# Performance work log

Hardware: AMD Instinct MI355X
Metric: run time of the kernel (lower is better)

The kernel has to match this reference:

```python
import jax, jax.numpy as jnp
import numpy as np

N_NODES = 200000
N_EDGES = 600000
N_GRAPHS = 4000
EMB = 128
LAYERS = 5
TASKS = 128
ATOM_FEATS, ATOM_VOCAB = 9, 64
BOND_FEATS, BOND_VOCAB = 3, 8
BN_EPS = 1e-5


def setup_inputs() -> dict:
    key = jax.random.key(0)
    ks = jax.random.split(key, 16)
    x = jax.random.randint(ks[0], (N_NODES, ATOM_FEATS), 0, ATOM_VOCAB)
    edge_index = jax.random.randint(ks[1], (2, N_EDGES), 0, N_NODES)
    edge_attr = jax.random.randint(ks[2], (N_EDGES, BOND_FEATS), 0, BOND_VOCAB)
    batch = jnp.sort(jax.random.randint(ks[3], (N_NODES,), 0, N_GRAPHS))
    s = 1.0 / np.sqrt(EMB)
    atom_emb = jax.random.normal(ks[4], (ATOM_FEATS, ATOM_VOCAB, EMB), jnp.float32) * s
    bond_emb = jax.random.normal(ks[5], (LAYERS, BOND_FEATS, BOND_VOCAB, EMB), jnp.float32) * s
    W = jax.random.normal(ks[6], (LAYERS, EMB, EMB), jnp.float32) * s
    b = jax.random.normal(ks[7], (LAYERS, EMB), jnp.float32) * 0.01
    root = jax.random.normal(ks[8], (LAYERS, EMB), jnp.float32) * s
    bn_mean = jax.random.normal(ks[9], (LAYERS, EMB), jnp.float32) * 0.1
    bn_var = jax.random.uniform(ks[10], (LAYERS, EMB), jnp.float32, 0.5, 1.5)
    bn_gamma = jax.random.uniform(ks[11], (LAYERS, EMB), jnp.float32, 0.5, 1.5)
    bn_beta = jax.random.normal(ks[12], (LAYERS, EMB), jnp.float32) * 0.1
    headW = jax.random.normal(ks[13], (EMB, TASKS), jnp.float32) * s
    headb = jnp.zeros((TASKS,), jnp.float32)
    return {"x": x, "edge_index": edge_index, "edge_attr": edge_attr, "batch": batch,
            "atom_emb": atom_emb, "bond_emb": bond_emb, "W": W, "b": b, "root": root,
            "bn_mean": bn_mean, "bn_var": bn_var, "bn_gamma": bn_gamma, "bn_beta": bn_beta,
            "headW": headW, "headb": headb}


def _gcn_forward(x, edge_index, edge_attr, batch, atom_emb, bond_emb, W, b, root,
                 bn_mean, bn_var, bn_gamma, bn_beta, headW, headb):
    src, dst = edge_index[0], edge_index[1]
    # AtomEncoder: sum of per-feature embeddings  -> [N, EMB]
    h = jnp.sum(jnp.take_along_axis(atom_emb, x.T[:, :, None], axis=1).squeeze(2), axis=0) \
        if False else sum(atom_emb[f][x[:, f]] for f in range(ATOM_FEATS))
    # degree of source nodes (+1 self loop), as in OGB GCNConv
    deg = jnp.zeros((N_NODES,), h.dtype).at[src].add(1.0) + 1.0
    dinv = deg ** -0.5
    norm = dinv[src] * dinv[dst]  # [E]
    for l in range(LAYERS):
        xl = h @ W[l] + b[l]
        edge_emb = sum(bond_emb[l, f][edge_attr[:, f]] for f in range(BOND_FEATS))  # [E, EMB]
        msg = norm[:, None] * jax.nn.relu(xl[src] + edge_emb)
        agg = jax.ops.segment_sum(msg, dst, num_segments=N_NODES)
        h = agg + jax.nn.relu(xl + root[l]) / deg[:, None]
        # BatchNorm1d (eval mode: running stats)
        h = (h - bn_mean[l]) * (bn_gamma[l] / jnp.sqrt(bn_var[l] + BN_EPS)) + bn_beta[l]
        if l != LAYERS - 1:
            h = jax.nn.relu(h)
        # dropout is identity in eval mode
    # global_add_pool over graphs
    hg = jax.ops.segment_sum(h, batch, num_segments=N_GRAPHS)
    return hg @ headW + headb


def reference(x, edge_index, edge_attr, batch, atom_emb, bond_emb, W, b, root,
              bn_mean, bn_var, bn_gamma, bn_beta, headW, headb):
    return _gcn_forward(x, edge_index, edge_attr, batch, atom_emb, bond_emb, W, b, root,
                        bn_mean, bn_var, bn_gamma, bn_beta, headW, headb)
```

## Files before the change

### kernel.cpp

```cpp
#include <hip/hip_runtime.h>
#include <hip/hip_bf16.h>

#define N_NODES 200000
#define N_EDGES 600000
#define N_GRAPHS 4000
#define EMB 128
#define LAYERS 5
#define BN_EPS 1e-5f

#define SCAN_CHUNK 2048
#define N_CHUNKS ((N_NODES + SCAN_CHUNK - 1) / SCAN_CHUNK)

typedef __attribute__((ext_vector_type(8))) short short8;
typedef __attribute__((ext_vector_type(8))) unsigned short ushort8v;
typedef __attribute__((ext_vector_type(4))) float float4v;

__device__ __forceinline__ void bf16split(float f, unsigned short& hi, unsigned short& lo) {
    unsigned u = __float_as_uint(f);
    hi = (unsigned short)(u >> 16);
    float hf = __uint_as_float((unsigned)hi << 16);
    lo = (unsigned short)(__float_as_uint(f - hf) >> 16);
}

__device__ __forceinline__ unsigned short f2bf_rne(float f) {
    unsigned u = __float_as_uint(f);
    u += 0x7FFF + ((u >> 16) & 1);
    return (unsigned short)(u >> 16);
}
__device__ __forceinline__ float bf2f(unsigned short h) {
    return __uint_as_float((unsigned)h << 16);
}

#define CNT_BLOCKS 2344
#define WP_BASE   CNT_BLOCKS
#define WP_BLOCKS 320
#define CB_BASE   (WP_BASE + WP_BLOCKS)
#define CB_BLOCKS 1280
#define BN_BASE   (CB_BASE + CB_BLOCKS)
#define BN_BLOCKS 3
#define GB_BASE   (BN_BASE + BN_BLOCKS)
#define GB_BLOCKS 16
#define AB_BASE   (GB_BASE + GB_BLOCKS)
#define AB_BLOCKS 288
#define PREP_BLOCKS (AB_BASE + AB_BLOCKS)

__global__ __launch_bounds__(256) void prep_all(
    const int* __restrict__ ei_src, const int* __restrict__ ei_dst,
    int* __restrict__ dsrc, int* __restrict__ ddst,
    const float* __restrict__ W, unsigned short* __restrict__ whi,
    unsigned short* __restrict__ wlo,
    const float* __restrict__ bemb, unsigned short* __restrict__ combo,
    const float* __restrict__ mean, const float* __restrict__ var,
    const float* __restrict__ gamma, const float* __restrict__ beta,
    float* __restrict__ S, float* __restrict__ T,
    const int* __restrict__ batch, int* __restrict__ gptr,
    const float* __restrict__ aemb, unsigned short* __restrict__ aembb) {
    const int b = blockIdx.x, tid = threadIdx.x;
    if (b < CNT_BLOCKS) {
        const int e = b * 256 + tid;
        if (e < N_EDGES) {
            atomicAdd(&dsrc[ei_src[e]], 1);
            atomicAdd(&ddst[ei_dst[e]], 1);
        }
    } else if (b < CB_BASE) {
        const int idx = (b - WP_BASE) * 256 + tid;
        const int l = idx >> 14, rem = idx & 16383;
        const int k = rem >> 7, n = rem & 127;
        unsigned short hi, lo;
        bf16split(W[idx], hi, lo);
        const int off = (l << 14) + ((((k >> 5) * 8 + (n >> 4)) * 64
                        + ((k >> 3) & 3) * 16 + (n & 15)) << 3) + (k & 7);
        whi[off] = hi;
        wlo[off] = lo;
    } else if (b < BN_BASE) {
        const int idx = (b - CB_BASE) * 256 + tid;
        const int l = idx >> 16;
        const int c = (idx >> 7) & 511;
        const int ch = idx & 127;
        const int a0 = c & 7, a1 = (c >> 3) & 7, a2 = c >> 6;
        combo[(size_t)(l * 512 + c) * EMB + ch] = f2bf_rne(
            bemb[(size_t)((l * 3 + 0) * 8 + a0) * EMB + ch] +
            bemb[(size_t)((l * 3 + 1) * 8 + a1) * EMB + ch] +
            bemb[(size_t)((l * 3 + 2) * 8 + a2) * EMB + ch]);
    } else if (b < GB_BASE) {
        const int i = (b - BN_BASE) * 256 + tid;
        if (i < LAYERS * EMB) {
            float s = gamma[i] / sqrtf(var[i] + BN_EPS);
            S[i] = s;
            T[i] = beta[i] - mean[i] * s;
        }
    } else if (b < AB_BASE) {
        const int g = (b - GB_BASE) * 256 + tid;
        if (g > N_GRAPHS) return;
        if (g == N_GRAPHS) { gptr[g] = N_NODES; return; }
        int lo = 0, hi = N_NODES;
        while (lo < hi) {
            int mid = (lo + hi) >> 1;
            if (batch[mid] < g) lo = mid + 1; else hi = mid;
        }
        gptr[g] = lo;
    } else {
        const int idx = (b - AB_BASE) * 256 + tid;
        aembb[idx] = f2bf_rne(aemb[idx]);
    }
}

__global__ __launch_bounds__(256) void scan1(const int* __restrict__ deg, int* __restrict__ partial) {
    __shared__ int sd[256];
    const int base = blockIdx.x * SCAN_CHUNK + threadIdx.x * 8;
    int s = 0;
#pragma unroll
    for (int i = 0; i < 8; ++i) { int idx = base + i; s += (idx < N_NODES) ? deg[idx] : 0; }
    sd[threadIdx.x] = s; __syncthreads();
    for (int off = 128; off > 0; off >>= 1) {
        if (threadIdx.x < off) sd[threadIdx.x] += sd[threadIdx.x + off];
        __syncthreads();
    }
    if (threadIdx.x == 0) partial[blockIdx.x] = sd[0];
}

__global__ __launch_bounds__(256) void scan3(const int* __restrict__ deg,
                                             const int* __restrict__ partial,
                                             int* __restrict__ rowptr) {
    __shared__ int sd[256];
    __shared__ int base_off;
    const int tid = threadIdx.x;
    if (tid == 0) {
        int acc = 0;
        for (int i = 0; i < (int)blockIdx.x; ++i) acc += partial[i];
        base_off = acc;
    }
    const int base = blockIdx.x * SCAN_CHUNK + tid * 8;
    int loc[8]; int s = 0;
#pragma unroll
    for (int i = 0; i < 8; ++i) { int idx = base + i; loc[i] = (idx < N_NODES) ? deg[idx] : 0; s += loc[i]; }
    sd[tid] = s; __syncthreads();
    for (int off = 1; off < 256; off <<= 1) {
        int v = (tid >= off) ? sd[tid - off] : 0;
        __syncthreads();
        sd[tid] += v;
        __syncthreads();
    }
    int excl = base_off + sd[tid] - s;
#pragma unroll
    for (int i = 0; i < 8; ++i) {
        int idx = base + i;
        if (idx < N_NODES) { rowptr[idx] = excl; excl += loc[i]; }
    }
    if (blockIdx.x == 0 && tid == 0) rowptr[N_NODES] = N_EDGES;
}

__global__ void scatter_k(const int* __restrict__ srcs, const int* __restrict__ dsts,
                          const int* __restrict__ eattr, const int* __restrict__ dsrc,
                          const int* __restrict__ rowptr, int* __restrict__ fill,
                          int* __restrict__ epk, float* __restrict__ enrm) {
    int e = blockIdx.x * blockDim.x + threadIdx.x;
    if (e >= N_EDGES) return;
    const int s = srcs[e];
    const int d = dsts[e];
    const int pos = rowptr[d] + atomicAdd(&fill[d], 1);
    const int c = eattr[e * 3] | (eattr[e * 3 + 1] << 3) | (eattr[e * 3 + 2] << 6);
    epk[pos] = s | (c << 18);
    enrm[pos] = rsqrtf((float)(dsrc[s] + 1) * (float)(dsrc[d] + 1));
}

__device__ __forceinline__ void mfma_tile64(
    unsigned short (*AhAl)[64][136],
    const short8* __restrict__ Bh, const short8* __restrict__ Bl,
    const float* __restrict__ bias, unsigned short* __restrict__ XLout,
    size_t rows, int tid) {
    const int wave = tid >> 6;
    const int lane = tid & 63;
    const int quad = lane >> 4;
    const int n15  = lane & 15;
    const int rt   = wave & 3;
    const int cp   = wave >> 2;
    const int arow = rt * 16 + n15;

    float4v acc0 = (float4v)(0.f);
    float4v acc1 = (float4v)(0.f);
#pragma unroll
    for (int ks = 0; ks < 4; ++ks) {
        const int k0 = ks * 32 + quad * 8;
        const short8 ah = *(const short8*)&AhAl[0][arow][k0];
        const short8 al = *(const short8*)&AhAl[1][arow][k0];
        const short8 bh0 = Bh[(ks * 8 + cp * 2 + 0) * 64 + lane];
        const short8 bl0 = Bl[(ks * 8 + cp * 2 + 0) * 64 + lane];
        const short8 bh1 = Bh[(ks * 8 + cp * 2 + 1) * 64 + lane];
        const short8 bl1 = Bl[(ks * 8 + cp * 2 + 1) * 64 + lane];
        acc0 = __builtin_amdgcn_mfma_f32_16x16x32_bf16(ah, bh0, acc0, 0, 0, 0);
        acc0 = __builtin_amdgcn_mfma_f32_16x16x32_bf16(ah, bl0, acc0, 0, 0, 0);
        acc0 = __builtin_amdgcn_mfma_f32_16x16x32_bf16(al, bh0, acc0, 0, 0, 0);
        acc1 = __builtin_amdgcn_mfma_f32_16x16x32_bf16(ah, bh1, acc1, 0, 0, 0);
        acc1 = __builtin_amdgcn_mfma_f32_16x16x32_bf16(ah, bl1, acc1, 0, 0, 0);
        acc1 = __builtin_amdgcn_mfma_f32_16x16x32_bf16(al, bh1, acc1, 0, 0, 0);
    }

    const size_t rowBase = rows + rt * 16 + quad * 4;
    const int col0 = (cp * 2 + 0) * 16 + n15;
    const int col1 = (cp * 2 + 1) * 16 + n15;
    const float bc0 = bias[col0];
    const float bc1 = bias[col1];
#pragma unroll
    for (int r = 0; r < 4; ++r) {
        XLout[(rowBase + r) * EMB + col0] = f2bf_rne(acc0[r] + bc0);
        XLout[(rowBase + r) * EMB + col1] = f2bf_rne(acc1[r] + bc1);
    }
}

__device__ __forceinline__ void mfma_tile16(
    unsigned short (*AhAl)[16][136],
    const short8* __restrict__ Bh, const short8* __restrict__ Bl,
    const float* __restrict__ bias, unsigned short* __restrict__ XLout,
    size_t rows, int tid) {
    const int wave = tid >> 6;
    const int lane = tid & 63;
    const int quad = lane >> 4;
    const int n15  = lane & 15;
    const int cp   = wave;
    const int arow = n15;

    float4v acc0 = (float4v)(0.f);
    float4v acc1 = (float4v)(0.f);
#pragma unroll
    for (int ks = 0; ks < 4; ++ks) {
        const int k0 = ks * 32 + quad * 8;
        const short8 ah = *(const short8*)&AhAl[0][arow][k0];
        const short8 al = *(const short8*)&AhAl[1][arow][k0];
        const short8 bh0 = Bh[(ks * 8 + cp * 2 + 0) * 64 + lane];
        const short8 bl0 = Bl[(ks * 8 + cp * 2 + 0) * 64 + lane];
        const short8 bh1 = Bh[(ks * 8 + cp * 2 + 1) * 64 + lane];
        const short8 bl1 = Bl[(ks * 8 + cp * 2 + 1) * 64 + lane];
        acc0 = __builtin_amdgcn_mfma_f32_16x16x32_bf16(ah, bh0, acc0, 0, 0, 0);
        acc0 = __builtin_amdgcn_mfma_f32_16x16x32_bf16(ah, bl0, acc0, 0, 0, 0);
        acc0 = __builtin_amdgcn_mfma_f32_16x16x32_bf16(al, bh0, acc0, 0, 0, 0);
        acc1 = __builtin_amdgcn_mfma_f32_16x16x32_bf16(ah, bh1, acc1, 0, 0, 0);
        acc1 = __builtin_amdgcn_mfma_f32_16x16x32_bf16(ah, bl1, acc1, 0, 0, 0);
        acc1 = __builtin_amdgcn_mfma_f32_16x16x32_bf16(al, bh1, acc1, 0, 0, 0);
    }

    const size_t rowBase = rows + quad * 4;
    const int col0 = (cp * 2 + 0) * 16 + n15;
    const int col1 = (cp * 2 + 1) * 16 + n15;
    const float bc0 = bias[col0];
    const float bc1 = bias[col1];
#pragma unroll
    for (int r = 0; r < 4; ++r) {
        XLout[(rowBase + r) * EMB + col0] = f2bf_rne(acc0[r] + bc0);
        XLout[(rowBase + r) * EMB + col1] = f2bf_rne(acc1[r] + bc1);
    }
}

__global__ __launch_bounds__(1024, 8) void enc_gemm(
    const int* __restrict__ x, const unsigned short* __restrict__ aembb,
    const unsigned short* __restrict__ whi, const unsigned short* __restrict__ wlo,
    const float* __restrict__ bias, unsigned short* __restrict__ XL) {
    __shared__ unsigned short AhAl[2][64][136];
    const int tid = threadIdx.x;
    const int q = tid & 15, qw = tid >> 4;
    const int c0 = q * 8;
    const size_t rows = (size_t)blockIdx.x * 64;

    {
        const size_t n = rows + qw;
        float4 a0 = make_float4(0.f, 0.f, 0.f, 0.f), a1 = a0;
#pragma unroll
        for (int ff = 0; ff < 9; ++ff) {
            const int v = x[n * 9 + ff];
            const ushort8v e = *(const ushort8v*)&aembb[(size_t)(ff * 64 + v) * EMB + c0];
            a0.x += bf2f(e[0]); a0.y += bf2f(e[1]);
            a0.z += bf2f(e[2]); a0.w += bf2f(e[3]);
            a1.x += bf2f(e[4]); a1.y += bf2f(e[5]);
            a1.z += bf2f(e[6]); a1.w += bf2f(e[7]);
        }
        ushort4 hi, lo;
        bf16split(a0.x, hi.x, lo.x); bf16split(a0.y, hi.y, lo.y);
        bf16split(a0.z, hi.z, lo.z); bf16split(a0.w, hi.w, lo.w);
        *(ushort4*)&AhAl[0][qw][c0] = hi;
        *(ushort4*)&AhAl[1][qw][c0] = lo;
        bf16split(a1.x, hi.x, lo.x); bf16split(a1.y, hi.y, lo.y);
        bf16split(a1.z, hi.z, lo.z); bf16split(a1.w, hi.w, lo.w);
        *(ushort4*)&AhAl[0][qw][c0 + 4] = hi;
        *(ushort4*)&AhAl[1][qw][c0 + 4] = lo;
    }
    __syncthreads();
    mfma_tile64(AhAl, (const short8*)whi, (const short8*)wlo, bias, XL, rows, tid);
}

__global__ __launch_bounds__(256, 8) void gather_gemm(
    const int* __restrict__ rowptr, const int* __restrict__ epk,
    const float* __restrict__ enrm, const unsigned short* __restrict__ combo,
    const float* __restrict__ root, const int* __restrict__ dsrc,
    const float* __restrict__ bnS, const float* __restrict__ bnT,
    const unsigned short* __restrict__ whi, const unsigned short* __restrict__ wlo,
    const float* __restrict__ bias,
    const unsigned short* __restrict__ XLin, unsigned short* __restrict__ XLout) {
    __shared__ unsigned short AhAl[2][16][136];
    const int tid = threadIdx.x;
    const int q = tid & 15, qw = tid >> 4;
    const int c0 = q * 8;
    const size_t rows = (size_t)blockIdx.x * 16;

    {
        const size_t n = rows + qw;
        const float4 r40 = *(const float4*)&root[c0];
        const float4 r41 = *(const float4*)&root[c0 + 4];
        const float4 s40 = *(const float4*)&bnS[c0];
        const float4 s41 = *(const float4*)&bnS[c0 + 4];
        const float4 t40 = *(const float4*)&bnT[c0];
        const float4 t41 = *(const float4*)&bnT[c0 + 4];
        const float dinv = 1.0f / (float)(dsrc[n] + 1);
        const ushort8v xn = *(const ushort8v*)&XLin[n * EMB + c0];
        float4 a0, a1;
        a0.x = fmaxf(bf2f(xn[0]) + r40.x, 0.f) * dinv;
        a0.y = fmaxf(bf2f(xn[1]) + r40.y, 0.f) * dinv;
        a0.z = fmaxf(bf2f(xn[2]) + r40.z, 0.f) * dinv;
        a0.w = fmaxf(bf2f(xn[3]) + r40.w, 0.f) * dinv;
        a1.x = fmaxf(bf2f(xn[4]) + r41.x, 0.f) * dinv;
        a1.y = fmaxf(bf2f(xn[5]) + r41.y, 0.f) * dinv;
        a1.z = fmaxf(bf2f(xn[6]) + r41.z, 0.f) * dinv;
        a1.w = fmaxf(bf2f(xn[7]) + r41.w, 0.f) * dinv;

        const int beg = rowptr[n], end = rowptr[n + 1];
        int pk = 0; float wgt = 0.f;
        if (beg < end) { pk = epk[beg]; wgt = enrm[beg]; }
        for (int e = beg; e < end; ++e) {
            const int pk_c = pk; const float w_c = wgt;
            if (e + 1 < end) { pk = epk[e + 1]; wgt = enrm[e + 1]; }
            const size_t sb = (size_t)(pk_c & 0x3FFFF) * EMB + c0;
            const size_t cbx = (size_t)(pk_c >> 18) * EMB + c0;
            const ushort8v xv = *(const ushort8v*)&XLin[sb];
            const ushort8v cb = *(const ushort8v*)&combo[cbx];
            a0.x += fmaxf(bf2f(xv[0]) + bf2f(cb[0]), 0.f) * w_c;
            a0.y += fmaxf(bf2f(xv[1]) + bf2f(cb[1]), 0.f) * w_c;
            a0.z += fmaxf(bf2f(xv[2]) + bf2f(cb[2]), 0.f) * w_c;
            a0.w += fmaxf(bf2f(xv[3]) + bf2f(cb[3]), 0.f) * w_c;
            a1.x += fmaxf(bf2f(xv[4]) + bf2f(cb[4]), 0.f) * w_c;
            a1.y += fmaxf(bf2f(xv[5]) + bf2f(cb[5]), 0.f) * w_c;
            a1.z += fmaxf(bf2f(xv[6]) + bf2f(cb[6]), 0.f) * w_c;
            a1.w += fmaxf(bf2f(xv[7]) + bf2f(cb[7]), 0.f) * w_c;
        }
        float4 h0, h1;
        h0.x = fmaxf(fmaf(a0.x, s40.x, t40.x), 0.f);
        h0.y = fmaxf(fmaf(a0.y, s40.y, t40.y), 0.f);
        h0.z = fmaxf(fmaf(a0.z, s40.z, t40.z), 0.f);
        h0.w = fmaxf(fmaf(a0.w, s40.w, t40.w), 0.f);
        h1.x = fmaxf(fmaf(a1.x, s41.x, t41.x), 0.f);
        h1.y = fmaxf(fmaf(a1.y, s41.y, t41.y), 0.f);
        h1.z = fmaxf(fmaf(a1.z, s41.z, t41.z), 0.f);
        h1.w = fmaxf(fmaf(a1.w, s41.w, t41.w), 0.f);
        ushort4 hi, lo;
        bf16split(h0.x, hi.x, lo.x); bf16split(h0.y, hi.y, lo.y);
        bf16split(h0.z, hi.z, lo.z); bf16split(h0.w, hi.w, lo.w);
        *(ushort4*)&AhAl[0][qw][c0] = hi;
        *(ushort4*)&AhAl[1][qw][c0] = lo;
        bf16split(h1.x, hi.x, lo.x); bf16split(h1.y, hi.y, lo.y);
        bf16split(h1.z, hi.z, lo.z); bf16split(h1.w, hi.w, lo.w);
        *(ushort4*)&AhAl[0][qw][c0 + 4] = hi;
        *(ushort4*)&AhAl[1][qw][c0 + 4] = lo;
    }
    __syncthreads();
    mfma_tile16(AhAl, (const short8*)whi, (const short8*)wlo, bias, XLout, rows, tid);
}

__global__ __launch_bounds__(512) void gather_pool_head(
    const int* __restrict__ rowptr, const int* __restrict__ epk,
    const float* __restrict__ enrm, const unsigned short* __restrict__ combo,
    const float* __restrict__ root, const int* __restrict__ dsrc,
    const float* __restrict__ S4, const float* __restrict__ T4,
    const int* __restrict__ gptr, const unsigned short* __restrict__ XLin,
    const float* __restrict__ HW, const float* __restrict__ hb,
    float* __restrict__ OUT) {
    __shared__ float red[32][EMB];
    __shared__ float hr[EMB];
    const int gph = blockIdx.x;
    const int q = threadIdx.x & 15, qw = threadIdx.x >> 4;
    const int c0 = q * 8;
    const int nbeg = gptr[gph], nend = gptr[gph + 1];
    const int ebeg = rowptr[nbeg], eend = rowptr[nend];

    const float4 r40 = *(const float4*)&root[c0];
    const float4 r41 = *(const float4*)&root[c0 + 4];

    float4 seg0 = make_float4(0.f, 0.f, 0.f, 0.f), seg1 = seg0;
    for (int n = nbeg + qw; n < nend; n += 32) {
        const float dinv = 1.0f / (float)(dsrc[n] + 1);
        const ushort8v xn = *(const ushort8v*)&XLin[(size_t)n * EMB + c0];
        seg0.x += fmaxf(bf2f(xn[0]) + r40.x, 0.f) * dinv;
        seg0.y += fmaxf(bf2f(xn[1]) + r40.y, 0.f) * dinv;
        seg0.z += fmaxf(bf2f(xn[2]) + r40.z, 0.f) * dinv;
        seg0.w += fmaxf(bf2f(xn[3]) + r40.w, 0.f) * dinv;
        seg1.x += fmaxf(bf2f(xn[4]) + r41.x, 0.f) * dinv;
        seg1.y += fmaxf(bf2f(xn[5]) + r41.y, 0.f) * dinv;
        seg1.z += fmaxf(bf2f(xn[6]) + r41.z, 0.f) * dinv;
        seg1.w += fmaxf(bf2f(xn[7]) + r41.w, 0.f) * dinv;
    }
    for (int i = ebeg + qw; i < eend; i += 32) {
        const int pk = epk[i];
        const float w = enrm[i];
        const size_t sb = (size_t)(pk & 0x3FFFF) * EMB + c0;
        const size_t cbx = (size_t)(pk >> 18) * EMB + c0;
        const ushort8v xv = *(const ushort8v*)&XLin[sb];
        const ushort8v cb = *(const ushort8v*)&combo[cbx];
        seg0.x += fmaxf(bf2f(xv[0]) + bf2f(cb[0]), 0.f) * w;
        seg0.y += fmaxf(bf2f(xv[1]) + bf2f(cb[1]), 0.f) * w;
        seg0.z += fmaxf(bf2f(xv[2]) + bf2f(cb[2]), 0.f) * w;
        seg0.w += fmaxf(bf2f(xv[3]) + bf2f(cb[3]), 0.f) * w;
        seg1.x += fmaxf(bf2f(xv[4]) + bf2f(cb[4]), 0.f) * w;
        seg1.y += fmaxf(bf2f(xv[5]) + bf2f(cb[5]), 0.f) * w;
        seg1.z += fmaxf(bf2f(xv[6]) + bf2f(cb[6]), 0.f) * w;
        seg1.w += fmaxf(bf2f(xv[7]) + bf2f(cb[7]), 0.f) * w;
    }
    *(float4*)&red[qw][c0] = seg0;
    *(float4*)&red[qw][c0 + 4] = seg1;
    __syncthreads();

    const int t = threadIdx.x;
    if (t < EMB) {
        float v = 0.f;
#pragma unroll
        for (int r = 0; r < 32; ++r) v += red[r][t];
        hr[t] = fmaf(v, S4[t], T4[t] * (float)(nend - nbeg));
    }
    __syncthreads();
    if (t < EMB) {
        float o = hb[t];
#pragma unroll 8
        for (int k = 0; k < EMB; ++k) o = fmaf(hr[k], HW[(size_t)k * EMB + t], o);
        OUT[(size_t)gph * EMB + t] = o;
    }
}

extern "C" void kernel_launch(void* const* d_in, const int* in_sizes, int n_in,
                              void* d_out, int out_size, void* d_ws, size_t ws_size,
                              hipStream_t stream) {
    const int*   x     = (const int*)d_in[0];
    const int*   ei    = (const int*)d_in[1];
    const int*   ea    = (const int*)d_in[2];
    const int*   batch = (const int*)d_in[3];
    const float* aemb  = (const float*)d_in[4];
    const float* bemb  = (const float*)d_in[5];
    const float* W     = (const float*)d_in[6];
    const float* b     = (const float*)d_in[7];
    const float* root  = (const float*)d_in[8];
    const float* bnm   = (const float*)d_in[9];
    const float* bnv   = (const float*)d_in[10];
    const float* bng   = (const float*)d_in[11];
    const float* bnb   = (const float*)d_in[12];
    const float* hW    = (const float*)d_in[13];
    const float* hb    = (const float*)d_in[14];
    float* out = (float*)d_out;

    const size_t NF = (size_t)N_NODES * EMB;
    const size_t n_float = NF + (size_t)LAYERS * 512 * EMB / 2
                         + 2 * LAYERS * EMB + N_EDGES
                         + 2 * ((size_t)LAYERS * 16384 / 2 + 64)
                         + (9 * 64 * EMB / 2 + 64);
    const size_t n_int   = 3 * (size_t)N_NODES + (N_NODES + 4) + 128
                         + (N_GRAPHS + 4) + N_EDGES;
    const size_t need = (n_float + n_int) * sizeof(float);
    if (ws_size < need) return;

    float* f     = (float*)d_ws;
    unsigned short* bufA = (unsigned short*)f; f += NF / 2;
    unsigned short* bufB = (unsigned short*)f; f += NF / 2;
    unsigned short* combo = (unsigned short*)f; f += (size_t)LAYERS * 512 * EMB / 2;
    float* S     = f;                          f += LAYERS * EMB;
    float* T     = f;                          f += LAYERS * EMB;
    float* enrm  = f;                          f += N_EDGES;
    unsigned short* whi = (unsigned short*)f;  f += (size_t)LAYERS * 16384 / 2 + 64;
    unsigned short* wlo = (unsigned short*)f;  f += (size_t)LAYERS * 16384 / 2 + 64;
    unsigned short* aembb = (unsigned short*)f; f += 9 * 64 * EMB / 2 + 64;
    int*   ip    = (int*)f;
    int*   dsrc    = ip;                       ip += N_NODES;
    int*   ddst    = ip;                       ip += N_NODES;
    int*   fill    = ip;                       ip += N_NODES;
    int*   rowptr  = ip;                       ip += N_NODES + 4;
    int*   partial = ip;                       ip += 128;
    int*   gptr    = ip;                       ip += N_GRAPHS + 4;
    int*   epk     = ip;                       ip += N_EDGES;

    hipMemsetAsync(dsrc, 0, 3 * (size_t)N_NODES * sizeof(int), stream);

    prep_all<<<PREP_BLOCKS, 256, 0, stream>>>(
        ei, ei + N_EDGES, dsrc, ddst, W, whi, wlo, bemb, combo,
        bnm, bnv, bng, bnb, S, T, batch, gptr, aemb, aembb);
    scan1<<<N_CHUNKS, 256, 0, stream>>>(ddst, partial);
    scan3<<<N_CHUNKS, 256, 0, stream>>>(ddst, partial, rowptr);
    scatter_k<<<(N_EDGES + 255) / 256, 256, 0, stream>>>(ei, ei + N_EDGES, ea, dsrc,
                                                         rowptr, fill, epk, enrm);

    enc_gemm<<<N_NODES / 64, 1024, 0, stream>>>(x, aembb, whi, wlo, b, bufA);

    unsigned short* in    = bufA;
    unsigned short* other = bufB;
    for (int l = 0; l < 4; ++l) {
        gather_gemm<<<N_NODES / 16, 256, 0, stream>>>(
            rowptr, epk, enrm, combo + (size_t)l * 512 * EMB, root + l * EMB, dsrc,
            S + l * EMB, T + l * EMB,
            whi + (size_t)(l + 1) * 16384, wlo + (size_t)(l + 1) * 16384,
            b + (l + 1) * EMB, in, other);
        unsigned short* t0 = in; in = other; other = t0;
    }

    gather_pool_head<<<N_GRAPHS, 512, 0, stream>>>(
        rowptr, epk, enrm, combo + (size_t)4 * 512 * EMB, root + 4 * EMB, dsrc,
        S + 4 * EMB, T + 4 * EMB, gptr, in, hW, hb, out);
}
```

Baseline: 544.5 us.

## Pack edge records into int2 and halve gather_gemm block to 128 threads

Edge source/attribute code and normalization weight are now stored together as one int2 record, so each edge needs a single 8-byte load instead of two separate array reads. The gather_gemm kernel now uses 128 threads per 16-row tile. Each thread covers 16 columns with two 16-byte loads per edge, and each of the two waves computes four 16-column MFMA tiles instead of two. The aim is fewer threads and fewer index loads per node, at the cost of more registers per thread and less parallelism per block.

```diff
diff --git a/kernel.cpp b/kernel.cpp
--- a/kernel.cpp
+++ b/kernel.cpp
@@ -153,15 +153,15 @@
 __global__ void scatter_k(const int* __restrict__ srcs, const int* __restrict__ dsts,
                           const int* __restrict__ eattr, const int* __restrict__ dsrc,
                           const int* __restrict__ rowptr, int* __restrict__ fill,
-                          int* __restrict__ epk, float* __restrict__ enrm) {
+                          int2* __restrict__ erec) {
     int e = blockIdx.x * blockDim.x + threadIdx.x;
     if (e >= N_EDGES) return;
     const int s = srcs[e];
     const int d = dsts[e];
     const int pos = rowptr[d] + atomicAdd(&fill[d], 1);
     const int c = eattr[e * 3] | (eattr[e * 3 + 1] << 3) | (eattr[e * 3 + 2] << 6);
-    epk[pos] = s | (c << 18);
-    enrm[pos] = rsqrtf((float)(dsrc[s] + 1) * (float)(dsrc[d] + 1));
+    const float nrm = rsqrtf((float)(dsrc[s] + 1) * (float)(dsrc[d] + 1));
+    erec[pos] = make_int2(s | (c << 18), __float_as_int(nrm));
 }
 
 __device__ __forceinline__ void mfma_tile64(
@@ -208,7 +208,7 @@
     }
 }
 
-__device__ __forceinline__ void mfma_tile16(
+__device__ __forceinline__ void mfma_tile16w2(
     unsigned short (*AhAl)[16][136],
     const short8* __restrict__ Bh, const short8* __restrict__ Bl,
     const float* __restrict__ bias, unsigned short* __restrict__ XLout,
@@ -217,37 +217,36 @@
     const int lane = tid & 63;
     const int quad = lane >> 4;
     const int n15  = lane & 15;
-    const int cp   = wave;
     const int arow = n15;
 
-    float4v acc0 = (float4v)(0.f);
-    float4v acc1 = (float4v)(0.f);
+    float4v acc[4];
+#pragma unroll
+    for (int j = 0; j < 4; ++j) acc[j] = (float4v)(0.f);
+
 #pragma unroll
     for (int ks = 0; ks < 4; ++ks) {
         const int k0 = ks * 32 + quad * 8;
         const short8 ah = *(const short8*)&AhAl[0][arow][k0];
         const short8 al = *(const short8*)&AhAl[1][arow][k0];
-        const short8 bh0 = Bh[(ks * 8 + cp * 2 + 0) * 64 + lane];
-        const short8 bl0 = Bl[(ks * 8 + cp * 2 + 0) * 64 + lane];
-        const short8 bh1 = Bh[(ks * 8 + cp * 2 + 1) * 64 + lane];
-        const short8 bl1 = Bl[(ks * 8 + cp * 2 + 1) * 64 + lane];
-        acc0 = __builtin_amdgcn_mfma_f32_16x16x32_bf16(ah, bh0, acc0, 0, 0, 0);
-        acc0 = __builtin_amdgcn_mfma_f32_16x16x32_bf16(ah, bl0, acc0, 0, 0, 0);
-        acc0 = __builtin_amdgcn_mfma_f32_16x16x32_bf16(al, bh0, acc0, 0, 0, 0);
-        acc1 = __builtin_amdgcn_mfma_f32_16x16x32_bf16(ah, bh1, acc1, 0, 0, 0);
-        acc1 = __builtin_amdgcn_mfma_f32_16x16x32_bf16(ah, bl1, acc1, 0, 0, 0);
-        acc1 = __builtin_amdgcn_mfma_f32_16x16x32_bf16(al, bh1, acc1, 0, 0, 0);
+#pragma unroll
+        for (int j = 0; j < 4; ++j) {
+            const int ct = wave * 4 + j;
+            const short8 bh = Bh[(ks * 8 + ct) * 64 + lane];
+            const short8 bl = Bl[(ks * 8 + ct) * 64 + lane];
+            acc[j] = __builtin_amdgcn_mfma_f32_16x16x32_bf16(ah, bh, acc[j], 0, 0, 0);
+            acc[j] = __builtin_amdgcn_mfma_f32_16x16x32_bf16(ah, bl, acc[j], 0, 0, 0);
+            acc[j] = __builtin_amdgcn_mfma_f32_16x16x32_bf16(al, bh, acc[j], 0, 0, 0);
+        }
     }
 
     const size_t rowBase = rows + quad * 4;
-    const int col0 = (cp * 2 + 0) * 16 + n15;
-    const int col1 = (cp * 2 + 1) * 16 + n15;
-    const float bc0 = bias[col0];
-    const float bc1 = bias[col1];
-#pragma unroll
-    for (int r = 0; r < 4; ++r) {
-        XLout[(rowBase + r) * EMB + col0] = f2bf_rne(acc0[r] + bc0);
-        XLout[(rowBase + r) * EMB + col1] = f2bf_rne(acc1[r] + bc1);
+#pragma unroll
+    for (int j = 0; j < 4; ++j) {
+        const int col = (wave * 4 + j) * 16 + n15;
+        const float bc = bias[col];
+#pragma unroll
+        for (int r = 0; r < 4; ++r)
+            XLout[(rowBase + r) * EMB + col] = f2bf_rne(acc[j][r] + bc);
     }
 }
 
@@ -287,9 +286,9 @@
     mfma_tile64(AhAl, (const short8*)whi, (const short8*)wlo, bias, XL, rows, tid);
 }
 
-__global__ __launch_bounds__(256, 8) void gather_gemm(
-    const int* __restrict__ rowptr, const int* __restrict__ epk,
-    const float* __restrict__ enrm, const unsigned short* __restrict__ combo,
+__global__ __launch_bounds__(128, 8) void gather_gemm(
+    const int* __restrict__ rowptr, const int2* __restrict__ erec,
+    const unsigned short* __restrict__ combo,
     const float* __restrict__ root, const int* __restrict__ dsrc,
     const float* __restrict__ bnS, const float* __restrict__ bnT,
     const unsigned short* __restrict__ whi, const unsigned short* __restrict__ wlo,
@@ -297,75 +296,113 @@
     const unsigned short* __restrict__ XLin, unsigned short* __restrict__ XLout) {
     __shared__ unsigned short AhAl[2][16][136];
     const int tid = threadIdx.x;
-    const int q = tid & 15, qw = tid >> 4;
-    const int c0 = q * 8;
+    const int o = tid & 7, qw = tid >> 3;
+    const int c0 = o * 16;
     const size_t rows = (size_t)blockIdx.x * 16;
 
     {
         const size_t n = rows + qw;
-        const float4 r40 = *(const float4*)&root[c0];
-        const float4 r41 = *(const float4*)&root[c0 + 4];
-        const float4 s40 = *(const float4*)&bnS[c0];
-        const float4 s41 = *(const float4*)&bnS[c0 + 4];
-        const float4 t40 = *(const float4*)&bnT[c0];
-        const float4 t41 = *(const float4*)&bnT[c0 + 4];
         const float dinv = 1.0f / (float)(dsrc[n] + 1);
-        const ushort8v xn = *(const ushort8v*)&XLin[n * EMB + c0];
-        float4 a0, a1;
-        a0.x = fmaxf(bf2f(xn[0]) + r40.x, 0.f) * dinv;
-        a0.y = fmaxf(bf2f(xn[1]) + r40.y, 0.f) * dinv;
-        a0.z = fmaxf(bf2f(xn[2]) + r40.z, 0.f) * dinv;
-        a0.w = fmaxf(bf2f(xn[3]) + r40.w, 0.f) * dinv;
-        a1.x = fmaxf(bf2f(xn[4]) + r41.x, 0.f) * dinv;
-        a1.y = fmaxf(bf2f(xn[5]) + r41.y, 0.f) * dinv;
-        a1.z = fmaxf(bf2f(xn[6]) + r41.z, 0.f) * dinv;
-        a1.w = fmaxf(bf2f(xn[7]) + r41.w, 0.f) * dinv;
+        float4 a0, a1, a2, a3;
+        {
+            const ushort8v xn0 = *(const ushort8v*)&XLin[n * EMB + c0];
+            const ushort8v xn1 = *(const ushort8v*)&XLin[n * EMB + c0 + 8];
+            const float4 r0 = *(const float4*)&root[c0];
+            const float4 r1 = *(const float4*)&root[c0 + 4];
+            const float4 r2 = *(const float4*)&root[c0 + 8];
+            const float4 r3 = *(const float4*)&root[c0 + 12];
+            a0.x = fmaxf(bf2f(xn0[0]) + r0.x, 0.f) * dinv;
+            a0.y = fmaxf(bf2f(xn0[1]) + r0.y, 0.f) * dinv;
+            a0.z = fmaxf(bf2f(xn0[2]) + r0.z, 0.f) * dinv;
+            a0.w = fmaxf(bf2f(xn0[3]) + r0.w, 0.f) * dinv;
+            a1.x = fmaxf(bf2f(xn0[4]) + r1.x, 0.f) * dinv;
+            a1.y = fmaxf(bf2f(xn0[5]) + r1.y, 0.f) * dinv;
+            a1.z = fmaxf(bf2f(xn0[6]) + r1.z, 0.f) * dinv;
+            a1.w = fmaxf(bf2f(xn0[7]) + r1.w, 0.f) * dinv;
+            a2.x = fmaxf(bf2f(xn1[0]) + r2.x, 0.f) * dinv;
+            a2.y = fmaxf(bf2f(xn1[1]) + r2.y, 0.f) * dinv;
+            a2.z = fmaxf(bf2f(xn1[2]) + r2.z, 0.f) * dinv;
+            a2.w = fmaxf(bf2f(xn1[3]) + r2.w, 0.f) * dinv;
+            a3.x = fmaxf(bf2f(xn1[4]) + r3.x, 0.f) * dinv;
+            a3.y = fmaxf(bf2f(xn1[5]) + r3.y, 0.f) * dinv;
+            a3.z = fmaxf(bf2f(xn1[6]) + r3.z, 0.f) * dinv;
+            a3.w = fmaxf(bf2f(xn1[7]) + r3.w, 0.f) * dinv;
+        }
 
         const int beg = rowptr[n], end = rowptr[n + 1];
-        int pk = 0; float wgt = 0.f;
-        if (beg < end) { pk = epk[beg]; wgt = enrm[beg]; }
+        int2 rec = make_int2(0, 0);
+        if (beg < end) rec = erec[beg];
         for (int e = beg; e < end; ++e) {
-            const int pk_c = pk; const float w_c = wgt;
-            if (e + 1 < end) { pk = epk[e + 1]; wgt = enrm[e + 1]; }
-            const size_t sb = (size_t)(pk_c & 0x3FFFF) * EMB + c0;
-            const size_t cbx = (size_t)(pk_c >> 18) * EMB + c0;
-            const ushort8v xv = *(const ushort8v*)&XLin[sb];
-            const ushort8v cb = *(const ushort8v*)&combo[cbx];
-            a0.x += fmaxf(bf2f(xv[0]) + bf2f(cb[0]), 0.f) * w_c;
-            a0.y += fmaxf(bf2f(xv[1]) + bf2f(cb[1]), 0.f) * w_c;
-            a0.z += fmaxf(bf2f(xv[2]) + bf2f(cb[2]), 0.f) * w_c;
-            a0.w += fmaxf(bf2f(xv[3]) + bf2f(cb[3]), 0.f) * w_c;
-            a1.x += fmaxf(bf2f(xv[4]) + bf2f(cb[4]), 0.f) * w_c;
-            a1.y += fmaxf(bf2f(xv[5]) + bf2f(cb[5]), 0.f) * w_c;
-            a1.z += fmaxf(bf2f(xv[6]) + bf2f(cb[6]), 0.f) * w_c;
-            a1.w += fmaxf(bf2f(xv[7]) + bf2f(cb[7]), 0.f) * w_c;
-        }
-        float4 h0, h1;
-        h0.x = fmaxf(fmaf(a0.x, s40.x, t40.x), 0.f);
-        h0.y = fmaxf(fmaf(a0.y, s40.y, t40.y), 0.f);
-        h0.z = fmaxf(fmaf(a0.z, s40.z, t40.z), 0.f);
-        h0.w = fmaxf(fmaf(a0.w, s40.w, t40.w), 0.f);
-        h1.x = fmaxf(fmaf(a1.x, s41.x, t41.x), 0.f);
-        h1.y = fmaxf(fmaf(a1.y, s41.y, t41.y), 0.f);
-        h1.z = fmaxf(fmaf(a1.z, s41.z, t41.z), 0.f);
-        h1.w = fmaxf(fmaf(a1.w, s41.w, t41.w), 0.f);
+            const int pk = rec.x;
+            const float w = __int_as_float(rec.y);
+            if (e + 1 < end) rec = erec[e + 1];
+            const size_t sb = (size_t)(pk & 0x3FFFF) * EMB + c0;
+            const size_t cbx = (size_t)(pk >> 18) * EMB + c0;
+            const ushort8v xv0 = *(const ushort8v*)&XLin[sb];
+            const ushort8v xv1 = *(const ushort8v*)&XLin[sb + 8];
+            const ushort8v cb0 = *(const ushort8v*)&combo[cbx];
+            const ushort8v cb1 = *(const ushort8v*)&combo[cbx + 8];
+            a0.x += fmaxf(bf2f(xv0[0]) + bf2f(cb0[0]), 0.f) * w;
+            a0.y += fmaxf(bf2f(xv0[1]) + bf2f(cb0[1]), 0.f) * w;
+            a0.z += fmaxf(bf2f(xv0[2]) + bf2f(cb0[2]), 0.f) * w;
+            a0.w += fmaxf(bf2f(xv0[3]) + bf2f(cb0[3]), 0.f) * w;
+            a1.x += fmaxf(bf2f(xv0[4]) + bf2f(cb0[4]), 0.f) * w;
+            a1.y += fmaxf(bf2f(xv0[5]) + bf2f(cb0[5]), 0.f) * w;
+            a1.z += fmaxf(bf2f(xv0[6]) + bf2f(cb0[6]), 0.f) * w;
+            a1.w += fmaxf(bf2f(xv0[7]) + bf2f(cb0[7]), 0.f) * w;
+            a2.x += fmaxf(bf2f(xv1[0]) + bf2f(cb1[0]), 0.f) * w;
+            a2.y += fmaxf(bf2f(xv1[1]) + bf2f(cb1[1]), 0.f) * w;
+            a2.z += fmaxf(bf2f(xv1[2]) + bf2f(cb1[2]), 0.f) * w;
+            a2.w += fmaxf(bf2f(xv1[3]) + bf2f(cb1[3]), 0.f) * w;
+            a3.x += fmaxf(bf2f(xv1[4]) + bf2f(cb1[4]), 0.f) * w;
+            a3.y += fmaxf(bf2f(xv1[5]) + bf2f(cb1[5]), 0.f) * w;
+            a3.z += fmaxf(bf2f(xv1[6]) + bf2f(cb1[6]), 0.f) * w;
+            a3.w += fmaxf(bf2f(xv1[7]) + bf2f(cb1[7]), 0.f) * w;
+        }
+
+        const float4 s0 = *(const float4*)&bnS[c0];
+        const float4 s1 = *(const float4*)&bnS[c0 + 4];
+        const float4 s2 = *(const float4*)&bnS[c0 + 8];
+        const float4 s3 = *(const float4*)&bnS[c0 + 12];
+        const float4 t0 = *(const float4*)&bnT[c0];
+        const float4 t1 = *(const float4*)&bnT[c0 + 4];
+        const float4 t2 = *(const float4*)&bnT[c0 + 8];
+        const float4 t3 = *(const float4*)&bnT[c0 + 12];
+        float h[16];
+        h[0]  = fmaxf(fmaf(a0.x, s0.x, t0.x), 0.f);
+        h[1]  = fmaxf(fmaf(a0.y, s0.y, t0.y), 0.f);
+        h[2]  = fmaxf(fmaf(a0.z, s0.z, t0.z), 0.f);
+        h[3]  = fmaxf(fmaf(a0.w, s0.w, t0.w), 0.f);
+        h[4]  = fmaxf(fmaf(a1.x, s1.x, t1.x), 0.f);
+        h[5]  = fmaxf(fmaf(a1.y, s1.y, t1.y), 0.f);
+        h[6]  = fmaxf(fmaf(a1.z, s1.z, t1.z), 0.f);
+        h[7]  = fmaxf(fmaf(a1.w, s1.w, t1.w), 0.f);
+        h[8]  = fmaxf(fmaf(a2.x, s2.x, t2.x), 0.f);
+        h[9]  = fmaxf(fmaf(a2.y, s2.y, t2.y), 0.f);
+        h[10] = fmaxf(fmaf(a2.z, s2.z, t2.z), 0.f);
+        h[11] = fmaxf(fmaf(a2.w, s2.w, t2.w), 0.f);
+        h[12] = fmaxf(fmaf(a3.x, s3.x, t3.x), 0.f);
+        h[13] = fmaxf(fmaf(a3.y, s3.y, t3.y), 0.f);
+        h[14] = fmaxf(fmaf(a3.z, s3.z, t3.z), 0.f);
+        h[15] = fmaxf(fmaf(a3.w, s3.w, t3.w), 0.f);
         ushort4 hi, lo;
-        bf16split(h0.x, hi.x, lo.x); bf16split(h0.y, hi.y, lo.y);
-        bf16split(h0.z, hi.z, lo.z); bf16split(h0.w, hi.w, lo.w);
-        *(ushort4*)&AhAl[0][qw][c0] = hi;
-        *(ushort4*)&AhAl[1][qw][c0] = lo;
-        bf16split(h1.x, hi.x, lo.x); bf16split(h1.y, hi.y, lo.y);
-        bf16split(h1.z, hi.z, lo.z); bf16split(h1.w, hi.w, lo.w);
-        *(ushort4*)&AhAl[0][qw][c0 + 4] = hi;
-        *(ushort4*)&AhAl[1][qw][c0 + 4] = lo;
+#pragma unroll
+        for (int g4 = 0; g4 < 4; ++g4) {
+            bf16split(h[g4 * 4 + 0], hi.x, lo.x);
+            bf16split(h[g4 * 4 + 1], hi.y, lo.y);
+            bf16split(h[g4 * 4 + 2], hi.z, lo.z);
+            bf16split(h[g4 * 4 + 3], hi.w, lo.w);
+            *(ushort4*)&AhAl[0][qw][c0 + g4 * 4] = hi;
+            *(ushort4*)&AhAl[1][qw][c0 + g4 * 4] = lo;
+        }
     }
     __syncthreads();
-    mfma_tile16(AhAl, (const short8*)whi, (const short8*)wlo, bias, XLout, rows, tid);
+    mfma_tile16w2(AhAl, (const short8*)whi, (const short8*)wlo, bias, XLout, rows, tid);
 }
 
 __global__ __launch_bounds__(512) void gather_pool_head(
-    const int* __restrict__ rowptr, const int* __restrict__ epk,
-    const float* __restrict__ enrm, const unsigned short* __restrict__ combo,
+    const int* __restrict__ rowptr, const int2* __restrict__ erec,
+    const unsigned short* __restrict__ combo,
     const float* __restrict__ root, const int* __restrict__ dsrc,
     const float* __restrict__ S4, const float* __restrict__ T4,
     const int* __restrict__ gptr, const unsigned short* __restrict__ XLin,
@@ -396,8 +433,9 @@
         seg1.w += fmaxf(bf2f(xn[7]) + r41.w, 0.f) * dinv;
     }
     for (int i = ebeg + qw; i < eend; i += 32) {
-        const int pk = epk[i];
-        const float w = enrm[i];
+        const int2 rec = erec[i];
+        const int pk = rec.x;
+        const float w = __int_as_float(rec.y);
         const size_t sb = (size_t)(pk & 0x3FFFF) * EMB + c0;
         const size_t cbx = (size_t)(pk >> 18) * EMB + c0;
         const ushort8v xv = *(const ushort8v*)&XLin[sb];
@@ -453,11 +491,12 @@
 
     const size_t NF = (size_t)N_NODES * EMB;
     const size_t n_float = NF + (size_t)LAYERS * 512 * EMB / 2
-                         + 2 * LAYERS * EMB + N_EDGES
+                         + 2 * LAYERS * EMB
                          + 2 * ((size_t)LAYERS * 16384 / 2 + 64)
                          + (9 * 64 * EMB / 2 + 64);
-    const size_t n_int   = 3 * (size_t)N_NODES + (N_NODES + 4) + 128
-                         + (N_GRAPHS + 4) + N_EDGES;
+    const size_t n_int   = 2 * (size_t)N_EDGES
+                         + 3 * (size_t)N_NODES + (N_NODES + 4) + 128
+                         + (N_GRAPHS + 4);
     const size_t need = (n_float + n_int) * sizeof(float);
     if (ws_size < need) return;
 
@@ -467,18 +506,17 @@
     unsigned short* combo = (unsigned short*)f; f += (size_t)LAYERS * 512 * EMB / 2;
     float* S     = f;                          f += LAYERS * EMB;
     float* T     = f;                          f += LAYERS * EMB;
-    float* enrm  = f;                          f += N_EDGES;
     unsigned short* whi = (unsigned short*)f;  f += (size_t)LAYERS * 16384 / 2 + 64;
     unsigned short* wlo = (unsigned short*)f;  f += (size_t)LAYERS * 16384 / 2 + 64;
     unsigned short* aembb = (unsigned short*)f; f += 9 * 64 * EMB / 2 + 64;
-    int*   ip    = (int*)f;
+    int2*  erec  = (int2*)f;
+    int*   ip    = (int*)(erec + N_EDGES);
     int*   dsrc    = ip;                       ip += N_NODES;
     int*   ddst    = ip;                       ip += N_NODES;
     int*   fill    = ip;                       ip += N_NODES;
     int*   rowptr  = ip;                       ip += N_NODES + 4;
     int*   partial = ip;                       ip += 128;
     int*   gptr    = ip;                       ip += N_GRAPHS + 4;
-    int*   epk     = ip;                       ip += N_EDGES;
 
     hipMemsetAsync(dsrc, 0, 3 * (size_t)N_NODES * sizeof(int), stream);
 
@@ -488,15 +526,15 @@
     scan1<<<N_CHUNKS, 256, 0, stream>>>(ddst, partial);
     scan3<<<N_CHUNKS, 256, 0, stream>>>(ddst, partial, rowptr);
     scatter_k<<<(N_EDGES + 255) / 256, 256, 0, stream>>>(ei, ei + N_EDGES, ea, dsrc,
-                                                         rowptr, fill, epk, enrm);
+                                                         rowptr, fill, erec);
 
     enc_gemm<<<N_NODES / 64, 1024, 0, stream>>>(x, aembb, whi, wlo, b, bufA);
 
     unsigned short* in    = bufA;
     unsigned short* other = bufB;
     for (int l = 0; l < 4; ++l) {
-        gather_gemm<<<N_NODES / 16, 256, 0, stream>>>(
-            rowptr, epk, enrm, combo + (size_t)l * 512 * EMB, root + l * EMB, dsrc,
+        gather_gemm<<<N_NODES / 16, 128, 0, stream>>>(
+            rowptr, erec, combo + (size_t)l * 512 * EMB, root + l * EMB, dsrc,
             S + l * EMB, T + l * EMB,
             whi + (size_t)(l + 1) * 16384, wlo + (size_t)(l + 1) * 16384,
             b + (l + 1) * EMB, in, other);
@@ -504,6 +542,6 @@
     }
 
     gather_pool_head<<<N_GRAPHS, 512, 0, stream>>>(
-        rowptr, epk, enrm, combo + (size_t)4 * 512 * EMB, root + 4 * EMB, dsrc,
+        rowptr, erec, combo + (size_t)4 * 512 * EMB, root + 4 * EMB, dsrc,
         S + 4 * EMB, T + 4 * EMB, gptr, in, hW, hb, out);
 }
```

After: 571.7 us. +5.0%, slower.
